# Kernel tuning notes

Measured on AMD Instinct MI355X. Metric: run time of the kernel, lower is better.

The kernel has to match this reference:

```python
import jax, jax.numpy as jnp
import numpy as np
from jax.scipy.special import logsumexp
from functools import partial

B, A, DIN, H, OUT, L = 256, 64, 512, 1024, 256, 3
HH = H // 2
SINKHORN_ITERS = 50
IDP = 0.1          # identity_preserve
SIG_BOUND = 1.0    # signal_bound
TEMP = 1.0
EPS = 1e-5


def setup_inputs() -> dict:
    key = jax.random.key(0)
    ks = iter(jax.random.split(key, 32))
    n = lambda shape, s=0.02: jax.random.normal(next(ks), shape, jnp.float32) * s
    return {
        'agent_states': jax.random.normal(next(ks), (B, A, DIN), jnp.float32),
        'Win': n((DIN, H), 0.03), 'bin_': jnp.zeros((H,), jnp.float32),
        # per-MHC-layer params, stacked over L
        'ln_g': jnp.ones((L, H), jnp.float32), 'ln_b': jnp.zeros((L, H), jnp.float32),
        'Wq': n((L, H, H)), 'bq': jnp.zeros((L, H), jnp.float32),
        'Wk': n((L, H, H)), 'bk': jnp.zeros((L, H), jnp.float32),
        'Wv': n((L, H, H)), 'bv': jnp.zeros((L, H), jnp.float32),
        'agent_biases': n((L, A, H)),
        'scale_factors': jnp.ones((L, A), jnp.float32),
        # inter-layer LayerNorms (L-1 of them)
        'iln_g': jnp.ones((L - 1, H), jnp.float32), 'iln_b': jnp.zeros((L - 1, H), jnp.float32),
        # per-agent output heads
        'W1': n((A, H, HH), 0.03), 'b1': jnp.zeros((A, HH), jnp.float32),
        'W2': n((A, HH, OUT), 0.03), 'b2': jnp.zeros((A, OUT), jnp.float32),
    }


def layer_norm(x, g, b):
    mu = jnp.mean(x, axis=-1, keepdims=True)
    var = jnp.mean(jnp.square(x - mu), axis=-1, keepdims=True)
    return (x - mu) * jax.lax.rsqrt(var + EPS) * g + b


def sinkhorn(log_alpha):
    # 50 alternating row/col log-space normalizations -> doubly stochastic
    def body(_, la):
        la = la - logsumexp(la, axis=2, keepdims=True)
        la = la - logsumexp(la, axis=1, keepdims=True)
        return la
    return jnp.exp(jax.lax.fori_loop(0, SINKHORN_ITERS, body, log_alpha))


def mhc_layer(h, ln_g, ln_b, Wq, bq, Wk, bk, Wv, bv, ab, sf):
    ns = layer_norm(h, ln_g, ln_b)                      # [B,A,H]
    q = ns @ Wq + bq
    k = ns @ Wk + bk
    v = ns @ Wv + bv
    scores = jnp.einsum('bad,bcd->bac', q, k) / (jnp.sqrt(jnp.float32(H)) * TEMP)
    attn = sinkhorn(scores)                              # [B,A,A]
    attended = jnp.einsum('bac,bcd->bad', attn, v)
    mixed = IDP * ns + (1.0 - IDP) * attended
    scaled = (mixed + ab) * sf[:, None]                  # bias + per-agent scale
    norms = jnp.linalg.norm(scaled, axis=2, keepdims=True)
    bounded = scaled / jnp.maximum(1.0, norms / SIG_BOUND)
    return h + bounded


def reference(agent_states, Win, bin_, ln_g, ln_b, Wq, bq, Wk, bk, Wv, bv,
              agent_biases, scale_factors, iln_g, iln_b, W1, b1, W2, b2):
    h = agent_states @ Win + bin_                        # input_proj (dropout=eval no-op)
    for i in range(L):
        h = mhc_layer(h, ln_g[i], ln_b[i], Wq[i], bq[i], Wk[i], bk[i],
                      Wv[i], bv[i], agent_biases[i], scale_factors[i])
        if i < L - 1:
            h = layer_norm(h, iln_g[i], iln_b[i])
    # per-agent MLP heads, vectorized over agents
    y = jnp.einsum('bah,aho->bao', h, W1) + b1
    y = jax.nn.gelu(y, approximate=False)
    out = jnp.einsum('bah,aho->bao', y, W2) + b2         # [B,A,OUT]
    return out
```

## Files before the change

kernel.cpp:

```cpp
#include <hip/hip_runtime.h>
#include <hip/hip_bf16.h>
#include <math.h>

#define BB 256
#define AA 64
#define DIN 512
#define HH_ 1024
#define HHALF 512
#define OUTD 256
#define LL 3
#define ROWS (BB * AA)
#define HN ((long)ROWS * HH_)

typedef float f32x4 __attribute__((ext_vector_type(4)));
typedef __bf16 bf16x8 __attribute__((ext_vector_type(8)));
typedef __bf16 bf16x4 __attribute__((ext_vector_type(4)));

__device__ __forceinline__ void gld_lds16(const void* g, void* l) {
    __builtin_amdgcn_global_load_lds(
        (const __attribute__((address_space(1))) unsigned int*)g,
        (__attribute__((address_space(3))) unsigned int*)l, 16, 0, 0);
}

#define TK 32
template <int ACT, int OUT_BF16, int SWZ>
__global__ __launch_bounds__(256) void mfma_gemm(
    const __bf16* __restrict__ Abase, const __bf16* __restrict__ Btbase,
    const float* __restrict__ biasBase, float* __restrict__ Cf,
    __bf16* __restrict__ Cb,
    int M, int N, int K, int lda, int ldb, int ldc,
    long sA, long sB, long sBias, long sC)
{
    const int z = blockIdx.z;
    const __bf16* A  = Abase  + (long)z * sA;
    const __bf16* Bt = Btbase + (long)z * sB;
    const float* bias = biasBase + (long)z * sBias;

    int bx = blockIdx.x, by = blockIdx.y;
    if (SWZ) {
        int lid = by * 24 + bx;
        int xcd = lid & 7, s = lid >> 3;
        by = (xcd >> 1) * 32 + s / 12;
        bx = (xcd & 1) * 12 + s % 12;
    }
    const int m0 = by * 128;
    const int n0 = bx * 128;

    __shared__ __bf16 sAt[128 * TK];
    __shared__ __bf16 sBt[128 * TK];

    const int t    = threadIdx.x;
    const int wv   = t >> 6;
    const int lane = t & 63;
    const int quad = lane >> 4;
    const int lrow = lane & 15;
    const int wm = (wv >> 1) * 64;
    const int wn = (wv & 1) * 64;

    f32x4 acc[4][4] = {};

    const int sr = t >> 2;
    const int sk = (t & 3) * 8;
    __bf16* la0 = sAt + wv * 512;
    __bf16* la1 = sAt + 64 * TK + wv * 512;
    __bf16* lb0 = sBt + wv * 512;
    __bf16* lb1 = sBt + 64 * TK + wv * 512;

    for (int k0 = 0; k0 < K; k0 += TK) {
        gld_lds16(A  + (long)(m0 + sr)      * lda + k0 + sk, la0);
        gld_lds16(A  + (long)(m0 + 64 + sr) * lda + k0 + sk, la1);
        gld_lds16(Bt + (long)(n0 + sr)      * ldb + k0 + sk, lb0);
        gld_lds16(Bt + (long)(n0 + 64 + sr) * ldb + k0 + sk, lb1);
        __syncthreads();

        bf16x8 af[4], bfr[4];
#pragma unroll
        for (int i = 0; i < 4; ++i)
            af[i] = *(const bf16x8*)(sAt + (wm + i * 16 + lrow) * TK + quad * 8);
#pragma unroll
        for (int j = 0; j < 4; ++j)
            bfr[j] = *(const bf16x8*)(sBt + (wn + j * 16 + lrow) * TK + quad * 8);
#pragma unroll
        for (int i = 0; i < 4; ++i)
#pragma unroll
            for (int j = 0; j < 4; ++j)
                acc[i][j] = __builtin_amdgcn_mfma_f32_16x16x32_bf16(
                    af[i], bfr[j], acc[i][j], 0, 0, 0);
        __syncthreads();
    }

#pragma unroll
    for (int i = 0; i < 4; ++i) {
#pragma unroll
        for (int p = 0; p < 4; ++p) {
            const int m = m0 + wm + i * 16 + quad * 4 + p;
#pragma unroll
            for (int j = 0; j < 4; ++j) {
                const int n = n0 + wn + j * 16 + lrow;
                float val = acc[i][j][p] + bias[n];
                if (ACT == 1) val = 0.5f * val * (1.0f + erff(val * 0.70710678118654752f));
                if (OUT_BF16) Cb[(long)z * sC + (long)m * ldc + n] = (__bf16)val;
                else          Cf[(long)z * sC + (long)m * ldc + n] = val;
            }
        }
    }
}

__global__ __launch_bounds__(256) void cast_kernel(
    const float* __restrict__ in, __bf16* __restrict__ out)
{
    long i = ((long)blockIdx.x * 256 + threadIdx.x) * 4;
    float4 v = *(const float4*)(in + i);
    bf16x4 o = {(__bf16)v.x, (__bf16)v.y, (__bf16)v.z, (__bf16)v.w};
    *(bf16x4*)(out + i) = o;
}

__global__ __launch_bounds__(256) void transpose_cast_kernel(
    const float* __restrict__ in, __bf16* __restrict__ out,
    int R, int C, long sIn, long sOut)
{
    const float* src = in + (long)blockIdx.z * sIn;
    __bf16* dst = out + (long)blockIdx.z * sOut;
    __shared__ float tile[32][33];
    const int r0 = blockIdx.y * 32, c0 = blockIdx.x * 32;
    const int tx = threadIdx.x & 31, ty = threadIdx.x >> 5;
#pragma unroll
    for (int i = 0; i < 32; i += 8)
        tile[ty + i][tx] = src[(long)(r0 + ty + i) * C + c0 + tx];
    __syncthreads();
#pragma unroll
    for (int i = 0; i < 32; i += 8)
        dst[(long)(c0 + ty + i) * R + r0 + tx] = (__bf16)tile[tx][ty + i];
}

__global__ __launch_bounds__(256) void qkv_bias_kernel(
    const float* __restrict__ bq, const float* __restrict__ bk,
    const float* __restrict__ bv, float* __restrict__ ob)
{
    int i = blockIdx.x * 256 + threadIdx.x;
    if (i >= LL * 3072) return;
    int l = i / 3072, j = i - l * 3072;
    float v = (j < 1024) ? bq[l * 1024 + j]
            : (j < 2048) ? bk[l * 1024 + j - 1024]
                         : bv[l * 1024 + j - 2048];
    ob[i] = v;
}

__global__ __launch_bounds__(256) void ln_kernel(
    const __bf16* __restrict__ x, const float* __restrict__ g,
    const float* __restrict__ b, __bf16* __restrict__ outb)
{
    __shared__ float s1[256], s2[256];
    const long row = blockIdx.x;
    const int t = threadIdx.x;
    bf16x4 vb = ((const bf16x4*)(x + row * HH_))[t];
    float4 v = {(float)vb[0], (float)vb[1], (float)vb[2], (float)vb[3]};
    s1[t] = v.x + v.y + v.z + v.w;
    s2[t] = v.x * v.x + v.y * v.y + v.z * v.z + v.w * v.w;
    __syncthreads();
    for (int off = 128; off > 0; off >>= 1) {
        if (t < off) { s1[t] += s1[t + off]; s2[t] += s2[t + off]; }
        __syncthreads();
    }
    float mu = s1[0] * (1.0f / 1024.0f);
    float var = s2[0] * (1.0f / 1024.0f) - mu * mu;
    float rstd = rsqrtf(var + 1e-5f);
    float4 gv = ((const float4*)g)[t];
    float4 bv = ((const float4*)b)[t];
    bf16x4 ob = {(__bf16)((v.x - mu) * rstd * gv.x + bv.x),
                 (__bf16)((v.y - mu) * rstd * gv.y + bv.y),
                 (__bf16)((v.z - mu) * rstd * gv.z + bv.z),
                 (__bf16)((v.w - mu) * rstd * gv.w + bv.w)};
    ((bf16x4*)(outb + row * HH_))[t] = ob;
}

__global__ __launch_bounds__(256) void attn_kernel(
    const __bf16* __restrict__ qkv, __bf16* __restrict__ att)
{
    const int z = blockIdx.x;
    __shared__ __bf16 sQ[64 * 32];
    __shared__ __bf16 sK[64 * 32];
    __shared__ float la[64 * 65];
    __shared__ float pm[4][64], ps[4][64];
    __shared__ __bf16 sP[64 * 68];
    __shared__ __bf16 sVT[64 * 68];

    const int t = threadIdx.x;
    const int wv = t >> 6, lane = t & 63;
    const int quad = lane >> 4, lrow = lane & 15;
    const int wm = (wv >> 1) * 32, wn = (wv & 1) * 32;

    {
        const int srow = t >> 2;
        const int skoff = (t & 3) * 8;
        __bf16* lq = sQ + wv * 512;
        __bf16* lk = sK + wv * 512;
        const __bf16* Q = qkv + (long)z * 64 * 3072;
        const __bf16* K = Q + 1024;

        f32x4 acc[2][2] = {};
        for (int k0 = 0; k0 < 1024; k0 += 32) {
            gld_lds16(Q + (long)srow * 3072 + k0 + skoff, lq);
            gld_lds16(K + (long)srow * 3072 + k0 + skoff, lk);
            __syncthreads();
            bf16x8 af[2], bfr[2];
#pragma unroll
            for (int i = 0; i < 2; ++i)
                af[i] = *(const bf16x8*)(sQ + (wm + i * 16 + lrow) * 32 + quad * 8);
#pragma unroll
            for (int j = 0; j < 2; ++j)
                bfr[j] = *(const bf16x8*)(sK + (wn + j * 16 + lrow) * 32 + quad * 8);
#pragma unroll
            for (int i = 0; i < 2; ++i)
#pragma unroll
                for (int j = 0; j < 2; ++j)
                    acc[i][j] = __builtin_amdgcn_mfma_f32_16x16x32_bf16(
                        af[i], bfr[j], acc[i][j], 0, 0, 0);
            __syncthreads();
        }
#pragma unroll
        for (int i = 0; i < 2; ++i)
#pragma unroll
            for (int p = 0; p < 4; ++p) {
                const int r = wm + i * 16 + quad * 4 + p;
#pragma unroll
                for (int j = 0; j < 2; ++j)
                    la[r * 65 + wn + j * 16 + lrow] = acc[i][j][p] * 0.03125f;
            }
        __syncthreads();
    }

    for (int it = 0; it < 50; ++it) {
        {
            float vr[16];
            float m = -INFINITY;
#pragma unroll
            for (int i = 0; i < 16; ++i) { vr[i] = la[lane * 65 + wv * 16 + i]; m = fmaxf(m, vr[i]); }
            float sum = 0.f;
#pragma unroll
            for (int i = 0; i < 16; ++i) sum += __expf(vr[i] - m);
            pm[wv][lane] = m; ps[wv][lane] = sum;
            __syncthreads();
            float m0 = pm[0][lane], m1 = pm[1][lane], m2 = pm[2][lane], m3 = pm[3][lane];
            float M = fmaxf(fmaxf(m0, m1), fmaxf(m2, m3));
            float S = ps[0][lane] * __expf(m0 - M) + ps[1][lane] * __expf(m1 - M)
                    + ps[2][lane] * __expf(m2 - M) + ps[3][lane] * __expf(m3 - M);
            float lse = M + __logf(S);
#pragma unroll
            for (int i = 0; i < 16; ++i) la[lane * 65 + wv * 16 + i] = vr[i] - lse;
            __syncthreads();
        }
        {
            float vr[16];
            float m = -INFINITY;
#pragma unroll
            for (int i = 0; i < 16; ++i) { vr[i] = la[(wv * 16 + i) * 65 + lane]; m = fmaxf(m, vr[i]); }
            float sum = 0.f;
#pragma unroll
            for (int i = 0; i < 16; ++i) sum += __expf(vr[i] - m);
            pm[wv][lane] = m; ps[wv][lane] = sum;
            __syncthreads();
            float m0 = pm[0][lane], m1 = pm[1][lane], m2 = pm[2][lane], m3 = pm[3][lane];
            float M = fmaxf(fmaxf(m0, m1), fmaxf(m2, m3));
            float S = ps[0][lane] * __expf(m0 - M) + ps[1][lane] * __expf(m1 - M)
                    + ps[2][lane] * __expf(m2 - M) + ps[3][lane] * __expf(m3 - M);
            float lse = M + __logf(S);
#pragma unroll
            for (int i = 0; i < 16; ++i) la[(wv * 16 + i) * 65 + lane] = vr[i] - lse;
            __syncthreads();
        }
    }

#pragma unroll
    for (int i = 0; i < 16; ++i) {
        int idx = t + i * 256;
        int r = idx >> 6, c = idx & 63;
        sP[r * 68 + c] = (__bf16)__expf(la[r * 65 + c]);
    }
    __syncthreads();

    const __bf16* V = qkv + (long)z * 64 * 3072 + 2048;
    const int vc = t >> 2;
    const int vn = (t & 3) * 16;
    for (int tile = 0; tile < 16; ++tile) {
        bf16x8 v0 = *(const bf16x8*)(V + (long)vc * 3072 + tile * 64 + vn);
        bf16x8 v1 = *(const bf16x8*)(V + (long)vc * 3072 + tile * 64 + vn + 8);
#pragma unroll
        for (int j = 0; j < 8; ++j) sVT[(vn + j) * 68 + vc] = v0[j];
#pragma unroll
        for (int j = 0; j < 8; ++j) sVT[(vn + 8 + j) * 68 + vc] = v1[j];
        __syncthreads();

        f32x4 pacc[2][2] = {};
#pragma unroll
        for (int kb = 0; kb < 2; ++kb) {
            bf16x8 af[2], bfr[2];
#pragma unroll
            for (int i = 0; i < 2; ++i) {
                const __bf16* p = sP + (wm + i * 16 + lrow) * 68 + kb * 32 + quad * 8;
                bf16x4 lo = *(const bf16x4*)p;
                bf16x4 hi = *(const bf16x4*)(p + 4);
                af[i] = bf16x8{lo[0], lo[1], lo[2], lo[3], hi[0], hi[1], hi[2], hi[3]};
            }
#pragma unroll
            for (int j = 0; j < 2; ++j) {
                const __bf16* p = sVT + (wn + j * 16 + lrow) * 68 + kb * 32 + quad * 8;
                bf16x4 lo = *(const bf16x4*)p;
                bf16x4 hi = *(const bf16x4*)(p + 4);
                bfr[j] = bf16x8{lo[0], lo[1], lo[2], lo[3], hi[0], hi[1], hi[2], hi[3]};
            }
#pragma unroll
            for (int i = 0; i < 2; ++i)
#pragma unroll
                for (int j = 0; j < 2; ++j)
                    pacc[i][j] = __builtin_amdgcn_mfma_f32_16x16x32_bf16(
                        af[i], bfr[j], pacc[i][j], 0, 0, 0);
        }
#pragma unroll
        for (int i = 0; i < 2; ++i)
#pragma unroll
            for (int p = 0; p < 4; ++p) {
                const int r = wm + i * 16 + quad * 4 + p;
#pragma unroll
                for (int j = 0; j < 2; ++j) {
                    const int n = tile * 64 + wn + j * 16 + lrow;
                    att[((long)z * 64 + r) * HH_ + n] = (__bf16)pacc[i][j][p];
                }
            }
        __syncthreads();
    }
}

__global__ __launch_bounds__(256) void mix_kernel(
    const __bf16* __restrict__ nsb_in, const __bf16* __restrict__ att,
    const float* __restrict__ ab, const float* __restrict__ sf,
    __bf16* __restrict__ h,
    const float* __restrict__ ig, const float* __restrict__ ib,
    const float* __restrict__ g2, const float* __restrict__ b2p, int doLN,
    __bf16* __restrict__ nsb_out)
{
    __shared__ float s1[256], s2[256];
    const long row = blockIdx.x;
    const int a = (int)(row & 63);
    const int t = threadIdx.x;

    bf16x4 nvb = ((const bf16x4*)(nsb_in + row * HH_))[t];
    bf16x4 avb = ((const bf16x4*)(att + row * HH_))[t];
    float4 abv = ((const float4*)(ab + (long)a * HH_))[t];
    float sfa = sf[a];

    float4 sc;
    sc.x = (0.1f * (float)nvb[0] + 0.9f * (float)avb[0] + abv.x) * sfa;
    sc.y = (0.1f * (float)nvb[1] + 0.9f * (float)avb[1] + abv.y) * sfa;
    sc.z = (0.1f * (float)nvb[2] + 0.9f * (float)avb[2] + abv.z) * sfa;
    sc.w = (0.1f * (float)nvb[3] + 0.9f * (float)avb[3] + abv.w) * sfa;

    s1[t] = sc.x * sc.x + sc.y * sc.y + sc.z * sc.z + sc.w * sc.w;
    __syncthreads();
    for (int off = 128; off > 0; off >>= 1) {
        if (t < off) s1[t] += s1[t + off];
        __syncthreads();
    }
    float norm = sqrtf(s1[0]);
    float inv = norm > 1.0f ? 1.0f / norm : 1.0f;

    bf16x4 hvb = ((const bf16x4*)(h + row * HH_))[t];
    float4 hn;
    hn.x = (float)hvb[0] + sc.x * inv;
    hn.y = (float)hvb[1] + sc.y * inv;
    hn.z = (float)hvb[2] + sc.z * inv;
    hn.w = (float)hvb[3] + sc.w * inv;

    if (!doLN) {
        bf16x4 ob = {(__bf16)hn.x, (__bf16)hn.y, (__bf16)hn.z, (__bf16)hn.w};
        ((bf16x4*)(h + row * HH_))[t] = ob;
        return;
    }
    __syncthreads();
    s1[t] = hn.x + hn.y + hn.z + hn.w;
    s2[t] = hn.x * hn.x + hn.y * hn.y + hn.z * hn.z + hn.w * hn.w;
    __syncthreads();
    for (int off = 128; off > 0; off >>= 1) {
        if (t < off) { s1[t] += s1[t + off]; s2[t] += s2[t + off]; }
        __syncthreads();
    }
    float mu = s1[0] * (1.0f / 1024.0f);
    float var = s2[0] * (1.0f / 1024.0f) - mu * mu;
    float rstd = rsqrtf(var + 1e-5f);
    float4 gv = ((const float4*)ig)[t];
    float4 bv = ((const float4*)ib)[t];
    hn.x = (hn.x - mu) * rstd * gv.x + bv.x;
    hn.y = (hn.y - mu) * rstd * gv.y + bv.y;
    hn.z = (hn.z - mu) * rstd * gv.z + bv.z;
    hn.w = (hn.w - mu) * rstd * gv.w + bv.w;
    bf16x4 ob = {(__bf16)hn.x, (__bf16)hn.y, (__bf16)hn.z, (__bf16)hn.w};
    ((bf16x4*)(h + row * HH_))[t] = ob;

    __syncthreads();
    s1[t] = hn.x + hn.y + hn.z + hn.w;
    s2[t] = hn.x * hn.x + hn.y * hn.y + hn.z * hn.z + hn.w * hn.w;
    __syncthreads();
    for (int off = 128; off > 0; off >>= 1) {
        if (t < off) { s1[t] += s1[t + off]; s2[t] += s2[t + off]; }
        __syncthreads();
    }
    mu = s1[0] * (1.0f / 1024.0f);
    var = s2[0] * (1.0f / 1024.0f) - mu * mu;
    rstd = rsqrtf(var + 1e-5f);
    float4 g2v = ((const float4*)g2)[t];
    float4 b2v = ((const float4*)b2p)[t];
    bf16x4 o2 = {(__bf16)((hn.x - mu) * rstd * g2v.x + b2v.x),
                 (__bf16)((hn.y - mu) * rstd * g2v.y + b2v.y),
                 (__bf16)((hn.z - mu) * rstd * g2v.z + b2v.z),
                 (__bf16)((hn.w - mu) * rstd * g2v.w + b2v.w)};
    ((bf16x4*)(nsb_out + row * HH_))[t] = o2;
}

extern "C" void kernel_launch(void* const* d_in, const int* in_sizes, int n_in,
                              void* d_out, int out_size, void* d_ws, size_t ws_size,
                              hipStream_t stream)
{
    const float* agent_states = (const float*)d_in[0];
    const float* Win   = (const float*)d_in[1];
    const float* bin_  = (const float*)d_in[2];
    const float* ln_g  = (const float*)d_in[3];
    const float* ln_b  = (const float*)d_in[4];
    const float* Wq    = (const float*)d_in[5];
    const float* bq    = (const float*)d_in[6];
    const float* Wk    = (const float*)d_in[7];
    const float* bk    = (const float*)d_in[8];
    const float* Wv    = (const float*)d_in[9];
    const float* bv    = (const float*)d_in[10];
    const float* ab    = (const float*)d_in[11];
    const float* sf    = (const float*)d_in[12];
    const float* ilg   = (const float*)d_in[13];
    const float* ilb   = (const float*)d_in[14];
    const float* W1    = (const float*)d_in[15];
    const float* b1    = (const float*)d_in[16];
    const float* W2    = (const float*)d_in[17];
    const float* b2    = (const float*)d_in[18];
    float* out = (float*)d_out;

    float* qbias = (float*)d_ws;
    __bf16* base = (__bf16*)(qbias + 16384);
    __bf16* nsb   = base;
    __bf16* h     = nsb + HN;
    __bf16* att   = h + HN;
    __bf16* qkvb  = att + HN;
    __bf16* Wqkvt = qkvb + 3 * HN;
    __bf16* asb  = att;
    __bf16* Wint = att + 8388608;
    __bf16* W1t = qkvb;
    __bf16* W2t = qkvb + 33554432;
    __bf16* yb  = qkvb + 41943040;

    cast_kernel<<<8192, 256, 0, stream>>>(agent_states, asb);
    transpose_cast_kernel<<<dim3(32, 16, 1), 256, 0, stream>>>(Win, Wint, 512, 1024, 0, 0);
    transpose_cast_kernel<<<dim3(32, 32, 3), 256, 0, stream>>>(Wq, Wqkvt,
                                                               1024, 1024, 1048576, 3145728);
    transpose_cast_kernel<<<dim3(32, 32, 3), 256, 0, stream>>>(Wk, Wqkvt + 1048576,
                                                               1024, 1024, 1048576, 3145728);
    transpose_cast_kernel<<<dim3(32, 32, 3), 256, 0, stream>>>(Wv, Wqkvt + 2097152,
                                                               1024, 1024, 1048576, 3145728);
    qkv_bias_kernel<<<36, 256, 0, stream>>>(bq, bk, bv, qbias);

    mfma_gemm<0, 1, 0><<<dim3(8, 128, 1), 256, 0, stream>>>(
        asb, Wint, bin_, nullptr, h, ROWS, HH_, DIN, DIN, DIN, HH_, 0, 0, 0, 0);
    ln_kernel<<<ROWS, 256, 0, stream>>>(h, ln_g, ln_b, nsb);

    for (int i = 0; i < LL; ++i) {
        mfma_gemm<0, 1, 1><<<dim3(24, 128, 1), 256, 0, stream>>>(
            nsb, Wqkvt + (long)i * 3145728, qbias + i * 3072, nullptr, qkvb,
            ROWS, 3072, HH_, HH_, HH_, 3072, 0, 0, 0, 0);
        attn_kernel<<<BB, 256, 0, stream>>>(qkvb, att);
        const int last = (i == LL - 1);
        mix_kernel<<<ROWS, 256, 0, stream>>>(
            nsb, att, ab + (long)i * AA * HH_, sf + i * AA, h,
            ilg + (last ? 0 : i) * HH_, ilb + (last ? 0 : i) * HH_,
            ln_g + (last ? 0 : (i + 1)) * HH_, ln_b + (last ? 0 : (i + 1)) * HH_,
            last ? 0 : 1, nsb);
    }

    transpose_cast_kernel<<<dim3(16, 32, 64), 256, 0, stream>>>(W1, W1t, 1024, 512,
                                                                524288, 524288);
    transpose_cast_kernel<<<dim3(8, 16, 64), 256, 0, stream>>>(W2, W2t, 512, 256,
                                                               131072, 131072);
    mfma_gemm<1, 1, 0><<<dim3(4, 2, 64), 256, 0, stream>>>(
        h, W1t, b1, nullptr, yb, BB, HHALF, HH_,
        AA * HH_, HH_, AA * HHALF, HH_, (long)HHALF * HH_, HHALF, HHALF);
    mfma_gemm<0, 0, 0><<<dim3(2, 2, 64), 256, 0, stream>>>(
        yb, W2t, b2, out, nullptr, BB, OUTD, HHALF,
        AA * HHALF, HHALF, AA * OUTD, HHALF, (long)OUTD * HHALF, OUTD, OUTD);
}
```

Before: 1.194 ms.

## Use wave-per-row shuffle reductions, fuse QKV transposes, drop Sinkhorn max-stabilization

LayerNorm and mix kernels now process one row per wavefront with register-held values and xor-shuffle reductions, replacing LDS tree reductions and repeated block barriers. The three Q/K/V weight transpose launches are merged into a single launch. The Sinkhorn loop drops the per-row/column max subtraction and directly sums exponentials, cutting exp and barrier-adjacent work per iteration but risking overflow if scores are large.

New measurement: 1.136 ms. -4.9%, faster.

```diff
diff --git a/kernel.cpp b/kernel.cpp
--- a/kernel.cpp
+++ b/kernel.cpp
@@ -133,6 +133,26 @@
         dst[(long)(c0 + ty + i) * R + r0 + tx] = (__bf16)tile[tx][ty + i];
 }
 
+__global__ __launch_bounds__(256) void transpose_qkv_kernel(
+    const float* __restrict__ Wq, const float* __restrict__ Wk,
+    const float* __restrict__ Wv, __bf16* __restrict__ out)
+{
+    const int zz = blockIdx.z;
+    const int layer = zz / 3, which = zz - layer * 3;
+    const float* src = (which == 0 ? Wq : which == 1 ? Wk : Wv) + (long)layer * 1048576;
+    __bf16* dst = out + (long)layer * 3145728 + (long)which * 1048576;
+    __shared__ float tile[32][33];
+    const int r0 = blockIdx.y * 32, c0 = blockIdx.x * 32;
+    const int tx = threadIdx.x & 31, ty = threadIdx.x >> 5;
+#pragma unroll
+    for (int i = 0; i < 32; i += 8)
+        tile[ty + i][tx] = src[(long)(r0 + ty + i) * 1024 + c0 + tx];
+    __syncthreads();
+#pragma unroll
+    for (int i = 0; i < 32; i += 8)
+        dst[(long)(c0 + ty + i) * 1024 + r0 + tx] = (__bf16)tile[tx][ty + i];
+}
+
 __global__ __launch_bounds__(256) void qkv_bias_kernel(
     const float* __restrict__ bq, const float* __restrict__ bk,
     const float* __restrict__ bv, float* __restrict__ ob)
@@ -150,28 +170,36 @@
     const __bf16* __restrict__ x, const float* __restrict__ g,
     const float* __restrict__ b, __bf16* __restrict__ outb)
 {
-    __shared__ float s1[256], s2[256];
-    const long row = blockIdx.x;
-    const int t = threadIdx.x;
-    bf16x4 vb = ((const bf16x4*)(x + row * HH_))[t];
-    float4 v = {(float)vb[0], (float)vb[1], (float)vb[2], (float)vb[3]};
-    s1[t] = v.x + v.y + v.z + v.w;
-    s2[t] = v.x * v.x + v.y * v.y + v.z * v.z + v.w * v.w;
-    __syncthreads();
-    for (int off = 128; off > 0; off >>= 1) {
-        if (t < off) { s1[t] += s1[t + off]; s2[t] += s2[t + off]; }
-        __syncthreads();
-    }
-    float mu = s1[0] * (1.0f / 1024.0f);
-    float var = s2[0] * (1.0f / 1024.0f) - mu * mu;
+    const int wv = threadIdx.x >> 6, lane = threadIdx.x & 63;
+    const long row = blockIdx.x * 4 + wv;
+    const __bf16* xr = x + row * HH_;
+    float v[16];
+    float s = 0.f, s2 = 0.f;
+#pragma unroll
+    for (int i = 0; i < 4; ++i) {
+        bf16x4 vb = *(const bf16x4*)(xr + i * 256 + lane * 4);
+#pragma unroll
+        for (int j = 0; j < 4; ++j) {
+            float f = (float)vb[j];
+            v[i * 4 + j] = f; s += f; s2 += f * f;
+        }
+    }
+#pragma unroll
+    for (int m = 1; m < 64; m <<= 1) { s += __shfl_xor(s, m); s2 += __shfl_xor(s2, m); }
+    float mu = s * (1.0f / 1024.0f);
+    float var = s2 * (1.0f / 1024.0f) - mu * mu;
     float rstd = rsqrtf(var + 1e-5f);
-    float4 gv = ((const float4*)g)[t];
-    float4 bv = ((const float4*)b)[t];
-    bf16x4 ob = {(__bf16)((v.x - mu) * rstd * gv.x + bv.x),
-                 (__bf16)((v.y - mu) * rstd * gv.y + bv.y),
-                 (__bf16)((v.z - mu) * rstd * gv.z + bv.z),
-                 (__bf16)((v.w - mu) * rstd * gv.w + bv.w)};
-    ((bf16x4*)(outb + row * HH_))[t] = ob;
+    __bf16* orow = outb + row * HH_;
+#pragma unroll
+    for (int i = 0; i < 4; ++i) {
+        float4 gv = *(const float4*)(g + i * 256 + lane * 4);
+        float4 bv = *(const float4*)(b + i * 256 + lane * 4);
+        bf16x4 ob = {(__bf16)((v[i*4+0] - mu) * rstd * gv.x + bv.x),
+                     (__bf16)((v[i*4+1] - mu) * rstd * gv.y + bv.y),
+                     (__bf16)((v[i*4+2] - mu) * rstd * gv.z + bv.z),
+                     (__bf16)((v[i*4+3] - mu) * rstd * gv.w + bv.w)};
+        *(bf16x4*)(orow + i * 256 + lane * 4) = ob;
+    }
 }
 
 __global__ __launch_bounds__(256) void attn_kernel(
@@ -181,7 +209,7 @@
     __shared__ __bf16 sQ[64 * 32];
     __shared__ __bf16 sK[64 * 32];
     __shared__ float la[64 * 65];
-    __shared__ float pm[4][64], ps[4][64];
+    __shared__ float ps[4][64];
     __shared__ __bf16 sP[64 * 68];
     __shared__ __bf16 sVT[64 * 68];
 
@@ -233,38 +261,28 @@
     for (int it = 0; it < 50; ++it) {
         {
             float vr[16];
-            float m = -INFINITY;
-#pragma unroll
-            for (int i = 0; i < 16; ++i) { vr[i] = la[lane * 65 + wv * 16 + i]; m = fmaxf(m, vr[i]); }
             float sum = 0.f;
 #pragma unroll
-            for (int i = 0; i < 16; ++i) sum += __expf(vr[i] - m);
-            pm[wv][lane] = m; ps[wv][lane] = sum;
+            for (int i = 0; i < 16; ++i) vr[i] = la[lane * 65 + wv * 16 + i];
+#pragma unroll
+            for (int i = 0; i < 16; ++i) sum += __expf(vr[i]);
+            ps[wv][lane] = sum;
             __syncthreads();
-            float m0 = pm[0][lane], m1 = pm[1][lane], m2 = pm[2][lane], m3 = pm[3][lane];
-            float M = fmaxf(fmaxf(m0, m1), fmaxf(m2, m3));
-            float S = ps[0][lane] * __expf(m0 - M) + ps[1][lane] * __expf(m1 - M)
-                    + ps[2][lane] * __expf(m2 - M) + ps[3][lane] * __expf(m3 - M);
-            float lse = M + __logf(S);
+            float lse = __logf(ps[0][lane] + ps[1][lane] + ps[2][lane] + ps[3][lane]);
 #pragma unroll
             for (int i = 0; i < 16; ++i) la[lane * 65 + wv * 16 + i] = vr[i] - lse;
             __syncthreads();
         }
         {
             float vr[16];
-            float m = -INFINITY;
-#pragma unroll
-            for (int i = 0; i < 16; ++i) { vr[i] = la[(wv * 16 + i) * 65 + lane]; m = fmaxf(m, vr[i]); }
             float sum = 0.f;
 #pragma unroll
-            for (int i = 0; i < 16; ++i) sum += __expf(vr[i] - m);
-            pm[wv][lane] = m; ps[wv][lane] = sum;
+            for (int i = 0; i < 16; ++i) vr[i] = la[(wv * 16 + i) * 65 + lane];
+#pragma unroll
+            for (int i = 0; i < 16; ++i) sum += __expf(vr[i]);
+            ps[wv][lane] = sum;
             __syncthreads();
-            float m0 = pm[0][lane], m1 = pm[1][lane], m2 = pm[2][lane], m3 = pm[3][lane];
-            float M = fmaxf(fmaxf(m0, m1), fmaxf(m2, m3));
-            float S = ps[0][lane] * __expf(m0 - M) + ps[1][lane] * __expf(m1 - M)
-                    + ps[2][lane] * __expf(m2 - M) + ps[3][lane] * __expf(m3 - M);
-            float lse = M + __logf(S);
+            float lse = __logf(ps[0][lane] + ps[1][lane] + ps[2][lane] + ps[3][lane]);
 #pragma unroll
             for (int i = 0; i < 16; ++i) la[(wv * 16 + i) * 65 + lane] = vr[i] - lse;
             __syncthreads();
@@ -339,81 +357,91 @@
     const float* __restrict__ g2, const float* __restrict__ b2p, int doLN,
     __bf16* __restrict__ nsb_out)
 {
-    __shared__ float s1[256], s2[256];
-    const long row = blockIdx.x;
+    const int wv = threadIdx.x >> 6, lane = threadIdx.x & 63;
+    const long row = blockIdx.x * 4 + wv;
     const int a = (int)(row & 63);
-    const int t = threadIdx.x;
-
-    bf16x4 nvb = ((const bf16x4*)(nsb_in + row * HH_))[t];
-    bf16x4 avb = ((const bf16x4*)(att + row * HH_))[t];
-    float4 abv = ((const float4*)(ab + (long)a * HH_))[t];
-    float sfa = sf[a];
-
-    float4 sc;
-    sc.x = (0.1f * (float)nvb[0] + 0.9f * (float)avb[0] + abv.x) * sfa;
-    sc.y = (0.1f * (float)nvb[1] + 0.9f * (float)avb[1] + abv.y) * sfa;
-    sc.z = (0.1f * (float)nvb[2] + 0.9f * (float)avb[2] + abv.z) * sfa;
-    sc.w = (0.1f * (float)nvb[3] + 0.9f * (float)avb[3] + abv.w) * sfa;
-
-    s1[t] = sc.x * sc.x + sc.y * sc.y + sc.z * sc.z + sc.w * sc.w;
-    __syncthreads();
-    for (int off = 128; off > 0; off >>= 1) {
-        if (t < off) s1[t] += s1[t + off];
-        __syncthreads();
-    }
-    float norm = sqrtf(s1[0]);
+    const float sfa = sf[a];
+
+    const __bf16* nr = nsb_in + row * HH_;
+    const __bf16* ar = att + row * HH_;
+    const float* abr = ab + (long)a * HH_;
+
+    float sc[16];
+    float nrm2 = 0.f;
+#pragma unroll
+    for (int i = 0; i < 4; ++i) {
+        bf16x4 nv = *(const bf16x4*)(nr + i * 256 + lane * 4);
+        bf16x4 av = *(const bf16x4*)(ar + i * 256 + lane * 4);
+        float4 a4 = *(const float4*)(abr + i * 256 + lane * 4);
+        float v0 = (0.1f * (float)nv[0] + 0.9f * (float)av[0] + a4.x) * sfa;
+        float v1 = (0.1f * (float)nv[1] + 0.9f * (float)av[1] + a4.y) * sfa;
+        float v2 = (0.1f * (float)nv[2] + 0.9f * (float)av[2] + a4.z) * sfa;
+        float v3 = (0.1f * (float)nv[3] + 0.9f * (float)av[3] + a4.w) * sfa;
+        sc[i*4+0] = v0; sc[i*4+1] = v1; sc[i*4+2] = v2; sc[i*4+3] = v3;
+        nrm2 += v0 * v0 + v1 * v1 + v2 * v2 + v3 * v3;
+    }
+#pragma unroll
+    for (int m = 1; m < 64; m <<= 1) nrm2 += __shfl_xor(nrm2, m);
+    float norm = sqrtf(nrm2);
     float inv = norm > 1.0f ? 1.0f / norm : 1.0f;
 
-    bf16x4 hvb = ((const bf16x4*)(h + row * HH_))[t];
-    float4 hn;
-    hn.x = (float)hvb[0] + sc.x * inv;
-    hn.y = (float)hvb[1] + sc.y * inv;
-    hn.z = (float)hvb[2] + sc.z * inv;
-    hn.w = (float)hvb[3] + sc.w * inv;
-
+    __bf16* hr = h + row * HH_;
+    float hn[16];
+    float s = 0.f, s2 = 0.f;
+#pragma unroll
+    for (int i = 0; i < 4; ++i) {
+        bf16x4 hv = *(const bf16x4*)(hr + i * 256 + lane * 4);
+#pragma unroll
+        for (int j = 0; j < 4; ++j) {
+            float f = (float)hv[j] + sc[i * 4 + j] * inv;
+            hn[i * 4 + j] = f; s += f; s2 += f * f;
+        }
+    }
     if (!doLN) {
-        bf16x4 ob = {(__bf16)hn.x, (__bf16)hn.y, (__bf16)hn.z, (__bf16)hn.w};
-        ((bf16x4*)(h + row * HH_))[t] = ob;
+#pragma unroll
+        for (int i = 0; i < 4; ++i) {
+            bf16x4 ob = {(__bf16)hn[i*4+0], (__bf16)hn[i*4+1],
+                         (__bf16)hn[i*4+2], (__bf16)hn[i*4+3]};
+            *(bf16x4*)(hr + i * 256 + lane * 4) = ob;
+        }
         return;
     }
-    __syncthreads();
-    s1[t] = hn.x + hn.y + hn.z + hn.w;
-    s2[t] = hn.x * hn.x + hn.y * hn.y + hn.z * hn.z + hn.w * hn.w;
-    __syncthreads();
-    for (int off = 128; off > 0; off >>= 1) {
-        if (t < off) { s1[t] += s1[t + off]; s2[t] += s2[t + off]; }
-        __syncthreads();
-    }
-    float mu = s1[0] * (1.0f / 1024.0f);
-    float var = s2[0] * (1.0f / 1024.0f) - mu * mu;
+#pragma unroll
+    for (int m = 1; m < 64; m <<= 1) { s += __shfl_xor(s, m); s2 += __shfl_xor(s2, m); }
+    float mu = s * (1.0f / 1024.0f);
+    float var = s2 * (1.0f / 1024.0f) - mu * mu;
     float rstd = rsqrtf(var + 1e-5f);
-    float4 gv = ((const float4*)ig)[t];
-    float4 bv = ((const float4*)ib)[t];
-    hn.x = (hn.x - mu) * rstd * gv.x + bv.x;
-    hn.y = (hn.y - mu) * rstd * gv.y + bv.y;
-    hn.z = (hn.z - mu) * rstd * gv.z + bv.z;
-    hn.w = (hn.w - mu) * rstd * gv.w + bv.w;
-    bf16x4 ob = {(__bf16)hn.x, (__bf16)hn.y, (__bf16)hn.z, (__bf16)hn.w};
-    ((bf16x4*)(h + row * HH_))[t] = ob;
-
-    __syncthreads();
-    s1[t] = hn.x + hn.y + hn.z + hn.w;
-    s2[t] = hn.x * hn.x + hn.y * hn.y + hn.z * hn.z + hn.w * hn.w;
-    __syncthreads();
-    for (int off = 128; off > 0; off >>= 1) {
-        if (t < off) { s1[t] += s1[t + off]; s2[t] += s2[t + off]; }
-        __syncthreads();
-    }
-    mu = s1[0] * (1.0f / 1024.0f);
-    var = s2[0] * (1.0f / 1024.0f) - mu * mu;
+    float s_1 = 0.f, s2_1 = 0.f;
+#pragma unroll
+    for (int i = 0; i < 4; ++i) {
+        float4 gv = *(const float4*)(ig + i * 256 + lane * 4);
+        float4 bv = *(const float4*)(ib + i * 256 + lane * 4);
+        float f0 = (hn[i*4+0] - mu) * rstd * gv.x + bv.x;
+        float f1 = (hn[i*4+1] - mu) * rstd * gv.y + bv.y;
+        float f2 = (hn[i*4+2] - mu) * rstd * gv.z + bv.z;
+        float f3 = (hn[i*4+3] - mu) * rstd * gv.w + bv.w;
+        hn[i*4+0] = f0; hn[i*4+1] = f1; hn[i*4+2] = f2; hn[i*4+3] = f3;
+        s_1 += f0 + f1 + f2 + f3;
+        s2_1 += f0 * f0 + f1 * f1 + f2 * f2 + f3 * f3;
+        bf16x4 ob = {(__bf16)f0, (__bf16)f1, (__bf16)f2, (__bf16)f3};
+        *(bf16x4*)(hr + i * 256 + lane * 4) = ob;
+    }
+#pragma unroll
+    for (int m = 1; m < 64; m <<= 1) { s_1 += __shfl_xor(s_1, m); s2_1 += __shfl_xor(s2_1, m); }
+    mu = s_1 * (1.0f / 1024.0f);
+    var = s2_1 * (1.0f / 1024.0f) - mu * mu;
     rstd = rsqrtf(var + 1e-5f);
-    float4 g2v = ((const float4*)g2)[t];
-    float4 b2v = ((const float4*)b2p)[t];
-    bf16x4 o2 = {(__bf16)((hn.x - mu) * rstd * g2v.x + b2v.x),
-                 (__bf16)((hn.y - mu) * rstd * g2v.y + b2v.y),
-                 (__bf16)((hn.z - mu) * rstd * g2v.z + b2v.z),
-                 (__bf16)((hn.w - mu) * rstd * g2v.w + b2v.w)};
-    ((bf16x4*)(nsb_out + row * HH_))[t] = o2;
+    __bf16* nor = nsb_out + row * HH_;
+#pragma unroll
+    for (int i = 0; i < 4; ++i) {
+        float4 gv = *(const float4*)(g2 + i * 256 + lane * 4);
+        float4 bv = *(const float4*)(b2p + i * 256 + lane * 4);
+        bf16x4 ob = {(__bf16)((hn[i*4+0] - mu) * rstd * gv.x + bv.x),
+                     (__bf16)((hn[i*4+1] - mu) * rstd * gv.y + bv.y),
+                     (__bf16)((hn[i*4+2] - mu) * rstd * gv.z + bv.z),
+                     (__bf16)((hn[i*4+3] - mu) * rstd * gv.w + bv.w)};
+        *(bf16x4*)(nor + i * 256 + lane * 4) = ob;
+    }
 }
 
 extern "C" void kernel_launch(void* const* d_in, const int* in_sizes, int n_in,
@@ -456,17 +484,12 @@
 
     cast_kernel<<<8192, 256, 0, stream>>>(agent_states, asb);
     transpose_cast_kernel<<<dim3(32, 16, 1), 256, 0, stream>>>(Win, Wint, 512, 1024, 0, 0);
-    transpose_cast_kernel<<<dim3(32, 32, 3), 256, 0, stream>>>(Wq, Wqkvt,
-                                                               1024, 1024, 1048576, 3145728);
-    transpose_cast_kernel<<<dim3(32, 32, 3), 256, 0, stream>>>(Wk, Wqkvt + 1048576,
-                                                               1024, 1024, 1048576, 3145728);
-    transpose_cast_kernel<<<dim3(32, 32, 3), 256, 0, stream>>>(Wv, Wqkvt + 2097152,
-                                                               1024, 1024, 1048576, 3145728);
+    transpose_qkv_kernel<<<dim3(32, 32, 9), 256, 0, stream>>>(Wq, Wk, Wv, Wqkvt);
     qkv_bias_kernel<<<36, 256, 0, stream>>>(bq, bk, bv, qbias);
 
     mfma_gemm<0, 1, 0><<<dim3(8, 128, 1), 256, 0, stream>>>(
         asb, Wint, bin_, nullptr, h, ROWS, HH_, DIN, DIN, DIN, HH_, 0, 0, 0, 0);
-    ln_kernel<<<ROWS, 256, 0, stream>>>(h, ln_g, ln_b, nsb);
+    ln_kernel<<<ROWS / 4, 256, 0, stream>>>(h, ln_g, ln_b, nsb);
 
     for (int i = 0; i < LL; ++i) {
         mfma_gemm<0, 1, 1><<<dim3(24, 128, 1), 256, 0, stream>>>(
@@ -474,7 +497,7 @@
             ROWS, 3072, HH_, HH_, HH_, 3072, 0, 0, 0, 0);
         attn_kernel<<<BB, 256, 0, stream>>>(qkvb, att);
         const int last = (i == LL - 1);
-        mix_kernel<<<ROWS, 256, 0, stream>>>(
+        mix_kernel<<<ROWS / 4, 256, 0, stream>>>(
             nsb, att, ab + (long)i * AA * HH_, sf + i * AA, h,
             ilg + (last ? 0 : i) * HH_, ilb + (last ? 0 : i) * HH_,
             ln_g + (last ? 0 : (i + 1)) * HH_, ln_b + (last ? 0 : (i + 1)) * HH_,
```
